# Kernel tuning notes

Hardware: AMD Instinct MI355X
Metric: run time of the kernel (lower is better)

The kernel has to match this reference:

```python
import jax, jax.numpy as jnp
import numpy as np

D_MODEL = 1024
NHEAD = 16
HEAD_DIM = D_MODEL // NHEAD
MAX_DIST = 128


def setup_inputs() -> dict:
    key = jax.random.key(0)
    ks = jax.random.split(key, 6)
    B, T = 2, 2048
    x = jax.random.normal(ks[0], (B, T, D_MODEL), dtype=jnp.float32)
    Wqkv = jax.random.normal(ks[1], (D_MODEL, 3 * D_MODEL), dtype=jnp.float32) * 0.02
    bqkv = jnp.zeros((3 * D_MODEL,), dtype=jnp.float32)
    Wout = jax.random.normal(ks[2], (D_MODEL, D_MODEL), dtype=jnp.float32) * 0.02
    bout = jnp.zeros((D_MODEL,), dtype=jnp.float32)
    rel_emb = jax.random.normal(ks[3], (2 * MAX_DIST + 1, NHEAD), dtype=jnp.float32) * 0.02
    return {"x": x, "Wqkv": Wqkv, "bqkv": bqkv, "Wout": Wout, "bout": bout, "rel_emb": rel_emb}


def _rel_bias(rel_emb, seq_len):
    pos = jnp.arange(seq_len)
    rel = pos[None, :] - pos[:, None]                       # [S,S]
    rel = jnp.clip(rel, -MAX_DIST, MAX_DIST) + MAX_DIST
    bias = rel_emb[rel]                                     # [S,S,H]
    bias = jnp.transpose(bias, (2, 0, 1))                   # [H,S,S]
    causal_mask = jnp.triu(jnp.ones((seq_len, seq_len), dtype=bool), k=1)
    return jnp.where(causal_mask[None, :, :], -jnp.inf, bias)


def reference(x, Wqkv, bqkv, Wout, bout, rel_emb):
    B, T, C = x.shape
    qkv = x @ Wqkv + bqkv                                   # [B,T,3C]
    q, k, v = jnp.split(qkv, 3, axis=-1)

    def split_heads(t):
        return jnp.transpose(t.reshape(B, T, NHEAD, HEAD_DIM), (0, 2, 1, 3))  # [B,H,T,Dh]

    q, k, v = split_heads(q), split_heads(k), split_heads(v)
    scale = jnp.sqrt(jnp.float32(HEAD_DIM))
    attn = jnp.einsum('bhtd,bhsd->bhts', q, k) / scale      # [B,H,T,S]
    bias = _rel_bias(rel_emb, T)                            # [H,T,S] (causal -inf mask baked in)
    attn = attn + bias[None, :, :, :]
    attn = jax.nn.softmax(attn, axis=-1)
    out = jnp.einsum('bhts,bhsd->bhtd', attn, v)            # [B,H,T,Dh]
    out = jnp.transpose(out, (0, 2, 1, 3)).reshape(B, T, C)
    return out @ Wout + bout
```

## Files before the change

### kernel.cpp

```cpp
#include <hip/hip_runtime.h>
#include <hip/hip_bf16.h>

typedef __attribute__((ext_vector_type(8))) short s8v;
typedef __attribute__((ext_vector_type(4))) float f4v;

__device__ __forceinline__ ushort f2bf(float f) {
    union { float f; unsigned u; } cv; cv.f = f;
    unsigned u = cv.u;
    unsigned lsb = (u >> 16) & 1u;
    u += 0x7fffu + lsb;
    return (ushort)(u >> 16);
}

typedef __attribute__((address_space(1))) void gvoid;
typedef __attribute__((address_space(3))) void lvoid;
__device__ __forceinline__ void gl_lds16(const ushort* g, ushort* l) {
    __builtin_amdgcn_global_load_lds((gvoid*)g, (lvoid*)l, 16, 0, 0);
}

__global__ void cast_bf16_kernel(const float* __restrict__ in, ushort* __restrict__ out, int n4) {
    int i = blockIdx.x * blockDim.x + threadIdx.x;
    if (i >= n4) return;
    float4 v = reinterpret_cast<const float4*>(in)[i];
    ushort4 o;
    o.x = f2bf(v.x); o.y = f2bf(v.y); o.z = f2bf(v.z); o.w = f2bf(v.w);
    reinterpret_cast<ushort4*>(out)[i] = o;
}

__global__ void transpose_cast_kernel(const float* __restrict__ in, ushort* __restrict__ out,
                                      int R, int C) {
    __shared__ float tile[32][33];
    int c0 = blockIdx.x * 32, r0 = blockIdx.y * 32;
    int tx = threadIdx.x & 31, ty = threadIdx.x >> 5;
    #pragma unroll
    for (int i = 0; i < 32; i += 8)
        tile[ty + i][tx] = in[(size_t)(r0 + ty + i) * C + c0 + tx];
    __syncthreads();
    #pragma unroll
    for (int i = 0; i < 32; i += 8)
        out[(size_t)(c0 + ty + i) * R + r0 + tx] = f2bf(tile[tx][ty + i]);
}

__global__ __launch_bounds__(256) void vtrans_kernel(
    const ushort* __restrict__ qkv, ushort* __restrict__ vt_g, int T)
{
    __shared__ ushort tile[64][72];
    const int sb = blockIdx.x * 64, bh = blockIdx.y;
    const int b = bh >> 4, h = bh & 15;
    const int t = threadIdx.x;
    const int r0 = t >> 3, c0 = (t & 7) * 8;
    const ushort* vsrc = qkv + (size_t)b * T * 3072 + 2048 + h * 64;
    *(s8v*)&tile[r0][c0]      = *(const s8v*)(vsrc + (size_t)(sb + r0) * 3072 + c0);
    *(s8v*)&tile[32 + r0][c0] = *(const s8v*)(vsrc + (size_t)(sb + 32 + r0) * 3072 + c0);
    __syncthreads();
    ushort* vdst = vt_g + (size_t)bh * 64 * T;
    s8v o0, o1;
    #pragma unroll
    for (int j = 0; j < 8; j++) {
        o0[j] = (short)tile[c0 + j][r0];
        o1[j] = (short)tile[c0 + j][32 + r0];
    }
    *(s8v*)(vdst + (size_t)r0 * T + sb + c0)        = o0;
    *(s8v*)(vdst + (size_t)(32 + r0) * T + sb + c0) = o1;
}

template <bool OUT_BF16>
__global__ __launch_bounds__(256) void gemm_bt_kernel(
    const ushort* __restrict__ A, const ushort* __restrict__ Bt,
    const float* __restrict__ bias, void* __restrict__ Cout,
    int M, int N, int K)
{
    __shared__ ushort As[128][64];
    __shared__ ushort Bs[128][64];
    const int t = threadIdx.x;
    const int m0 = blockIdx.y * 128, n0 = blockIdx.x * 128;
    const int wave = t >> 6, lane = t & 63;
    const int lr = lane & 15, lg = lane >> 4;
    const int wm = (wave >> 1) * 64, wn = (wave & 1) * 64;
    const int lrow = lane >> 3;
    const int lcol = (lane & 7) * 8;

    f4v acc[4][4];
    #pragma unroll
    for (int i = 0; i < 4; i++)
        #pragma unroll
        for (int j = 0; j < 4; j++)
            acc[i][j] = (f4v){0.f, 0.f, 0.f, 0.f};

    for (int k0 = 0; k0 < K; k0 += 64) {
        __syncthreads();
        #pragma unroll
        for (int i = 0; i < 4; i++) {
            int j = wave * 4 + i;
            int row = j * 8 + lrow;
            gl_lds16(A  + (size_t)(m0 + row) * K + k0 + lcol, &As[j * 8][0]);
            gl_lds16(Bt + (size_t)(n0 + row) * K + k0 + lcol, &Bs[j * 8][0]);
        }
        __syncthreads();
        #pragma unroll
        for (int ks = 0; ks < 64; ks += 32) {
            s8v af[4], bfr[4];
            #pragma unroll
            for (int mb = 0; mb < 4; mb++)
                af[mb] = *reinterpret_cast<const s8v*>(&As[wm + mb * 16 + lr][ks + lg * 8]);
            #pragma unroll
            for (int nb = 0; nb < 4; nb++)
                bfr[nb] = *reinterpret_cast<const s8v*>(&Bs[wn + nb * 16 + lr][ks + lg * 8]);
            #pragma unroll
            for (int mb = 0; mb < 4; mb++)
                #pragma unroll
                for (int nb = 0; nb < 4; nb++)
                    acc[mb][nb] = __builtin_amdgcn_mfma_f32_16x16x32_bf16(af[mb], bfr[nb], acc[mb][nb], 0, 0, 0);
        }
    }

    #pragma unroll
    for (int mb = 0; mb < 4; mb++) {
        #pragma unroll
        for (int nb = 0; nb < 4; nb++) {
            int col = n0 + wn + nb * 16 + lr;
            float bv = bias[col];
            #pragma unroll
            for (int r = 0; r < 4; r++) {
                int row = m0 + wm + mb * 16 + lg * 4 + r;
                float val = acc[mb][nb][r] + bv;
                if (OUT_BF16)
                    reinterpret_cast<ushort*>(Cout)[(size_t)row * N + col] = f2bf(val);
                else
                    reinterpret_cast<float*>(Cout)[(size_t)row * N + col] = val;
            }
        }
    }
}

__device__ __forceinline__ void attn_tile_sw(
    const s8v qf0, const s8v qf1, int q_abs, int qb, int sb,
    int lr, int lg,
    const ushort (*Ks)[72], const ushort (*Vs)[72],
    ushort (*pT)[72],
    const float* rel_lds,
    float& m, float& l, f4v* oT)
{
    const float SC = 0.125f * 1.44269504f;
    f4v sacc[4];
    __builtin_amdgcn_s_setprio(1);
    #pragma unroll
    for (int cb = 0; cb < 4; cb++) {
        sacc[cb] = (f4v){0.f, 0.f, 0.f, 0.f};
        s8v kf0 = *(const s8v*)&Ks[cb * 16 + lr][lg * 8];
        s8v kf1 = *(const s8v*)&Ks[cb * 16 + lr][32 + lg * 8];
        sacc[cb] = __builtin_amdgcn_mfma_f32_16x16x32_bf16(kf0, qf0, sacc[cb], 0, 0, 0);
        sacc[cb] = __builtin_amdgcn_mfma_f32_16x16x32_bf16(kf1, qf1, sacc[cb], 0, 0, 0);
    }
    __builtin_amdgcn_s_setprio(0);

    if (sb + 192 <= qb) {
        float c = rel_lds[0];
        #pragma unroll
        for (int cb = 0; cb < 4; cb++)
            #pragma unroll
            for (int r = 0; r < 4; r++)
                sacc[cb][r] = sacc[cb][r] * SC + c;
    } else {
        #pragma unroll
        for (int cb = 0; cb < 4; cb++) {
            #pragma unroll
            for (int r = 0; r < 4; r++) {
                int s = sb + cb * 16 + lg * 4 + r;
                int rel = s - q_abs;
                rel = (rel < -128 ? -128 : (rel > 128 ? 128 : rel)) + 128;
                float val = sacc[cb][r] * SC + rel_lds[rel];
                if (s > q_abs) val = -3.0e38f;
                sacc[cb][r] = val;
            }
        }
    }

    float pm0 = fmaxf(fmaxf(sacc[0][0], sacc[0][1]), fmaxf(sacc[0][2], sacc[0][3]));
    float pm1 = fmaxf(fmaxf(sacc[1][0], sacc[1][1]), fmaxf(sacc[1][2], sacc[1][3]));
    float pm2 = fmaxf(fmaxf(sacc[2][0], sacc[2][1]), fmaxf(sacc[2][2], sacc[2][3]));
    float pm3 = fmaxf(fmaxf(sacc[3][0], sacc[3][1]), fmaxf(sacc[3][2], sacc[3][3]));
    float pm = fmaxf(fmaxf(pm0, pm1), fmaxf(pm2, pm3));
    pm = fmaxf(pm, __shfl_xor(pm, 16, 64));
    pm = fmaxf(pm, __shfl_xor(pm, 32, 64));

    if (__any(pm > m + 8.0f)) {
        float mnew = fmaxf(m, pm);
        float alpha = exp2f(m - mnew);
        l *= alpha;
        #pragma unroll
        for (int d = 0; d < 4; d++)
            #pragma unroll
            for (int r = 0; r < 4; r++)
                oT[d][r] *= alpha;
        m = mnew;
    }

    float sum = 0.f;
    #pragma unroll
    for (int cb = 0; cb < 4; cb++) {
        #pragma unroll
        for (int r = 0; r < 4; r++) {
            float p = exp2f(sacc[cb][r] - m);
            sacc[cb][r] = p;
            sum += p;
        }
    }
    sum += __shfl_xor(sum, 16, 64);
    sum += __shfl_xor(sum, 32, 64);
    l += sum;

    #pragma unroll
    for (int cb = 0; cb < 4; cb++) {
        unsigned lo = (unsigned)f2bf(sacc[cb][0]) | ((unsigned)f2bf(sacc[cb][1]) << 16);
        unsigned hi = (unsigned)f2bf(sacc[cb][2]) | ((unsigned)f2bf(sacc[cb][3]) << 16);
        *(unsigned long long*)&pT[lr][cb * 16 + lg * 4] =
            (unsigned long long)lo | ((unsigned long long)hi << 32);
    }

    __builtin_amdgcn_s_setprio(1);
    #pragma unroll
    for (int ch = 0; ch < 2; ch++) {
        s8v pf = *(const s8v*)&pT[lr][ch * 32 + lg * 8];
        #pragma unroll
        for (int d = 0; d < 4; d++) {
            s8v vf = *(const s8v*)&Vs[d * 16 + lr][ch * 32 + lg * 8];
            oT[d] = __builtin_amdgcn_mfma_f32_16x16x32_bf16(vf, pf, oT[d], 0, 0, 0);
        }
    }
    __builtin_amdgcn_s_setprio(0);
}

__device__ __forceinline__ void store_O(
    f4v* oT, float l, int lr, int lg, int lane, int qrow0,
    ushort (*pT)[72], size_t rowb, int h, ushort* __restrict__ attn_out)
{
    float inv = 1.0f / l;
    #pragma unroll
    for (int d = 0; d < 4; d++) {
        unsigned lo = (unsigned)f2bf(oT[d][0] * inv) | ((unsigned)f2bf(oT[d][1] * inv) << 16);
        unsigned hi = (unsigned)f2bf(oT[d][2] * inv) | ((unsigned)f2bf(oT[d][3] * inv) << 16);
        *(unsigned long long*)&pT[lr][d * 16 + lg * 4] =
            (unsigned long long)lo | ((unsigned long long)hi << 32);
    }
    int q_r = lane >> 2, part = lane & 3;
    s8v a = *(const s8v*)&pT[q_r][part * 16];
    s8v b = *(const s8v*)&pT[q_r][part * 16 + 8];
    ushort* dst = attn_out + (rowb + qrow0 + q_r) * 1024 + h * 64 + part * 16;
    *(s8v*)dst = a;
    *(s8v*)(dst + 8) = b;
}

__global__ __launch_bounds__(256, 4) void attn_kernel(
    const ushort* __restrict__ qkv, const ushort* __restrict__ vt_g,
    const float* __restrict__ rel_emb, ushort* __restrict__ attn_out, int T)
{
    __shared__ ushort Ks[64][72];
    __shared__ ushort Vs[64][72];
    __shared__ ushort p_lds[4][16][72];
    __shared__ float rel_lds[257];

    const int t = threadIdx.x;
    const int bh = blockIdx.y;
    const int p = (blockIdx.x + bh) & 31;
    const int lo = p, hi = 63 - p;
    const int b = bh >> 4, h = bh & 15;
    const size_t rowb = (size_t)b * T;

    for (int i = t; i < 257; i += 256) rel_lds[i] = rel_emb[i * 16 + h] * 1.44269504f;

    const int wave = t >> 6, lane = t & 63;
    const int lr = lane & 15, lg = lane >> 4;
    const int sr = t >> 3, sc = (t & 7) * 8;

    const int my_tile = (wave < 2) ? hi : lo;
    const int qtb = my_tile * 32;
    const int qrow0 = qtb + (wave & 1) * 16;
    const int qa = qrow0 + lr;
    const int my_nt = (qtb + 31) / 64 + 1;
    const int ntH = ((63 - p) * 32 + 31) / 64 + 1;

    const ushort* kbase = qkv + rowb * 3072 + 1024 + h * 64;
    const ushort* vbase = vt_g + (size_t)bh * 64 * T;

    const ushort* qptr = qkv + (rowb + qa) * 3072 + h * 64;
    s8v qf0 = *(const s8v*)(qptr + lg * 8);
    s8v qf1 = *(const s8v*)(qptr + 32 + lg * 8);

    float m = -3.0e38f, l = 0.f;
    f4v oT[4];
    #pragma unroll
    for (int d = 0; d < 4; d++) oT[d] = (f4v){0.f, 0.f, 0.f, 0.f};

    s8v ka0 = *(const s8v*)(kbase + (size_t)sr * 3072 + sc);
    s8v ka1 = *(const s8v*)(kbase + (size_t)(32 + sr) * 3072 + sc);
    s8v va0 = *(const s8v*)(vbase + (size_t)sr * T + sc);
    s8v va1 = *(const s8v*)(vbase + (size_t)(32 + sr) * T + sc);

    for (int st = 0; st < ntH; ++st) {
        const int sb = st * 64;
        __syncthreads();
        *(s8v*)&Ks[sr][sc]      = ka0;
        *(s8v*)&Ks[32 + sr][sc] = ka1;
        *(s8v*)&Vs[sr][sc]      = va0;
        *(s8v*)&Vs[32 + sr][sc] = va1;
        __syncthreads();

        if (st + 1 < ntH) {
            const int sn = sb + 64;
            ka0 = *(const s8v*)(kbase + (size_t)(sn + sr) * 3072 + sc);
            ka1 = *(const s8v*)(kbase + (size_t)(sn + 32 + sr) * 3072 + sc);
            va0 = *(const s8v*)(vbase + (size_t)sr * T + sn + sc);
            va1 = *(const s8v*)(vbase + (size_t)(32 + sr) * T + sn + sc);
        }

        if (st < my_nt)
            attn_tile_sw(qf0, qf1, qa, qtb, sb, lr, lg, Ks, Vs, p_lds[wave], rel_lds, m, l, oT);
    }

    store_O(oT, l, lr, lg, lane, qrow0, p_lds[wave], rowb, h, attn_out);
}

extern "C" void kernel_launch(void* const* d_in, const int* in_sizes, int n_in,
                              void* d_out, int out_size, void* d_ws, size_t ws_size,
                              hipStream_t stream) {
    const float* x       = (const float*)d_in[0];
    const float* Wqkv    = (const float*)d_in[1];
    const float* bqkv    = (const float*)d_in[2];
    const float* Wout    = (const float*)d_in[3];
    const float* bout    = (const float*)d_in[4];
    const float* rel_emb = (const float*)d_in[5];
    float* out = (float*)d_out;

    const int M = in_sizes[0] / 1024;
    const int T = 2048;
    const int B = M / T;

    ushort* x_bf = (ushort*)d_ws;
    ushort* Wq_t = x_bf + (size_t)M * 1024;
    ushort* Wo_t = Wq_t + (size_t)3072 * 1024;
    ushort* qkv  = Wo_t + (size_t)1024 * 1024;
    ushort* attn = qkv + (size_t)M * 3072;
    ushort* vt_g = attn + (size_t)M * 1024;

    hipLaunchKernelGGL(cast_bf16_kernel, dim3((M * 1024 / 4 + 255) / 256), dim3(256), 0, stream,
                       x, x_bf, M * 1024 / 4);
    hipLaunchKernelGGL(transpose_cast_kernel, dim3(3072 / 32, 1024 / 32), dim3(256), 0, stream,
                       Wqkv, Wq_t, 1024, 3072);
    hipLaunchKernelGGL(transpose_cast_kernel, dim3(1024 / 32, 1024 / 32), dim3(256), 0, stream,
                       Wout, Wo_t, 1024, 1024);
    hipLaunchKernelGGL((gemm_bt_kernel<true>), dim3(3072 / 128, M / 128), dim3(256), 0, stream,
                       x_bf, Wq_t, bqkv, (void*)qkv, M, 3072, 1024);
    hipLaunchKernelGGL(vtrans_kernel, dim3(T / 64, B * 16), dim3(256), 0, stream,
                       qkv, vt_g, T);
    hipLaunchKernelGGL(attn_kernel, dim3(32, B * 16), dim3(256), 0, stream,
                       qkv, vt_g, rel_emb, attn, T);
    hipLaunchKernelGGL((gemm_bt_kernel<false>), dim3(1024 / 128, M / 128), dim3(256), 0, stream,
                       attn, Wo_t, bout, (void*)out, M, 1024, 1024);
}
```

Baseline: 234.4 us.

## Replace paired causal q-tile balancing with 1D grid scheduling heaviest tiles first

Result: faster. 220.5 us (-5.9%).

```diff
diff --git a/kernel.cpp b/kernel.cpp
--- a/kernel.cpp
+++ b/kernel.cpp
@@ -232,8 +232,8 @@
 }
 
 __device__ __forceinline__ void store_O(
-    f4v* oT, float l, int lr, int lg, int lane, int qrow0,
-    ushort (*pT)[72], size_t rowb, int h, ushort* __restrict__ attn_out)
+    f4v* oT, float l, int lr, int lg, int lane, int wave,
+    ushort (*pT)[72], int qb, size_t rowb, int h, ushort* __restrict__ attn_out)
 {
     float inv = 1.0f / l;
     #pragma unroll
@@ -246,7 +246,7 @@
     int q_r = lane >> 2, part = lane & 3;
     s8v a = *(const s8v*)&pT[q_r][part * 16];
     s8v b = *(const s8v*)&pT[q_r][part * 16 + 8];
-    ushort* dst = attn_out + (rowb + qrow0 + q_r) * 1024 + h * 64 + part * 16;
+    ushort* dst = attn_out + (rowb + qb + wave * 16 + q_r) * 1024 + h * 64 + part * 16;
     *(s8v*)dst = a;
     *(s8v*)(dst + 8) = b;
 }
@@ -261,9 +261,10 @@
     __shared__ float rel_lds[257];
 
     const int t = threadIdx.x;
-    const int bh = blockIdx.y;
-    const int p = (blockIdx.x + bh) & 31;
-    const int lo = p, hi = 63 - p;
+    const int x = blockIdx.x;
+    const int qt = 31 - (x >> 5);
+    const int bh = x & 31;
+    const int qb = qt * 64;
     const int b = bh >> 4, h = bh & 15;
     const size_t rowb = (size_t)b * T;
 
@@ -273,16 +274,10 @@
     const int lr = lane & 15, lg = lane >> 4;
     const int sr = t >> 3, sc = (t & 7) * 8;
 
-    const int my_tile = (wave < 2) ? hi : lo;
-    const int qtb = my_tile * 32;
-    const int qrow0 = qtb + (wave & 1) * 16;
-    const int qa = qrow0 + lr;
-    const int my_nt = (qtb + 31) / 64 + 1;
-    const int ntH = ((63 - p) * 32 + 31) / 64 + 1;
-
     const ushort* kbase = qkv + rowb * 3072 + 1024 + h * 64;
     const ushort* vbase = vt_g + (size_t)bh * 64 * T;
 
+    const int qa = qb + wave * 16 + lr;
     const ushort* qptr = qkv + (rowb + qa) * 3072 + h * 64;
     s8v qf0 = *(const s8v*)(qptr + lg * 8);
     s8v qf1 = *(const s8v*)(qptr + 32 + lg * 8);
@@ -291,13 +286,15 @@
     f4v oT[4];
     #pragma unroll
     for (int d = 0; d < 4; d++) oT[d] = (f4v){0.f, 0.f, 0.f, 0.f};
+
+    const int nt = qt + 1;
 
     s8v ka0 = *(const s8v*)(kbase + (size_t)sr * 3072 + sc);
     s8v ka1 = *(const s8v*)(kbase + (size_t)(32 + sr) * 3072 + sc);
     s8v va0 = *(const s8v*)(vbase + (size_t)sr * T + sc);
     s8v va1 = *(const s8v*)(vbase + (size_t)(32 + sr) * T + sc);
 
-    for (int st = 0; st < ntH; ++st) {
+    for (int st = 0; st < nt; ++st) {
         const int sb = st * 64;
         __syncthreads();
         *(s8v*)&Ks[sr][sc]      = ka0;
@@ -306,7 +303,7 @@
         *(s8v*)&Vs[32 + sr][sc] = va1;
         __syncthreads();
 
-        if (st + 1 < ntH) {
+        if (st + 1 < nt) {
             const int sn = sb + 64;
             ka0 = *(const s8v*)(kbase + (size_t)(sn + sr) * 3072 + sc);
             ka1 = *(const s8v*)(kbase + (size_t)(sn + 32 + sr) * 3072 + sc);
@@ -314,11 +311,10 @@
             va1 = *(const s8v*)(vbase + (size_t)(32 + sr) * T + sn + sc);
         }
 
-        if (st < my_nt)
-            attn_tile_sw(qf0, qf1, qa, qtb, sb, lr, lg, Ks, Vs, p_lds[wave], rel_lds, m, l, oT);
-    }
-
-    store_O(oT, l, lr, lg, lane, qrow0, p_lds[wave], rowb, h, attn_out);
+        attn_tile_sw(qf0, qf1, qa, qb, sb, lr, lg, Ks, Vs, p_lds[wave], rel_lds, m, l, oT);
+    }
+
+    store_O(oT, l, lr, lg, lane, wave, p_lds[wave], qb, rowb, h, attn_out);
 }
 
 extern "C" void kernel_launch(void* const* d_in, const int* in_sizes, int n_in,
@@ -353,7 +349,7 @@
                        x_bf, Wq_t, bqkv, (void*)qkv, M, 3072, 1024);
     hipLaunchKernelGGL(vtrans_kernel, dim3(T / 64, B * 16), dim3(256), 0, stream,
                        qkv, vt_g, T);
-    hipLaunchKernelGGL(attn_kernel, dim3(32, B * 16), dim3(256), 0, stream,
+    hipLaunchKernelGGL(attn_kernel, dim3(32 * B * 16), dim3(256), 0, stream,
                        qkv, vt_g, rel_emb, attn, T);
     hipLaunchKernelGGL((gemm_bt_kernel<false>), dim3(1024 / 128, M / 128), dim3(256), 0, stream,
                        attn, Wo_t, bout, (void*)out, M, 1024, 1024);
```
